# Optimization experiments

Hardware: AMD Instinct MI355X
Metric: run time of the kernel (lower is better)

Reference implementation:

```python
import jax, jax.numpy as jnp
import numpy as np

B, T, J, D, H = 64, 240, 22, 128, 8


def setup_inputs() -> dict:
    key = jax.random.key(0)
    ks = jax.random.split(key, 6)
    x = jax.random.normal(ks[0], (B, T, J, D), dtype=jnp.float32)
    adjacency = jax.random.randint(ks[1], (J, J), 0, 2, dtype=jnp.int32)
    # self-loops so no softmax row is fully masked (matches sane graph usage)
    adjacency = adjacency.at[jnp.arange(J), jnp.arange(J)].set(1)
    in_proj_w = jax.random.normal(ks[2], (3 * D, D), dtype=jnp.float32) * 0.05
    in_proj_b = jax.random.normal(ks[3], (3 * D,), dtype=jnp.float32) * 0.02
    out_w = jax.random.normal(ks[4], (D, D), dtype=jnp.float32) * 0.05
    out_b = jax.random.normal(ks[5], (D,), dtype=jnp.float32) * 0.02
    return {"x": x, "adjacency": adjacency, "in_proj_w": in_proj_w,
            "in_proj_b": in_proj_b, "out_w": out_w, "out_b": out_b}


def reference(x, adjacency, in_proj_w, in_proj_b, out_w, out_b):
    b, t, j, d = x.shape
    hd = d // H
    n = b * t
    x_bt = x.reshape(n, j, d)
    # combined QKV projection (nn.MultiheadAttention in_proj)
    qkv = x_bt @ in_proj_w.T + in_proj_b            # [n, j, 3d]
    q, k, v = jnp.split(qkv, 3, axis=-1)
    split_heads = lambda a: a.reshape(n, j, H, hd).transpose(0, 2, 1, 3)  # [n,H,j,hd]
    q, k, v = split_heads(q), split_heads(k), split_heads(v)
    scores = jnp.einsum('nhqd,nhkd->nhqk', q, k) / np.sqrt(hd).astype(np.float32)
    mask = adjacency <= 0                            # True = disallowed (bool attn_mask)
    scores = jnp.where(mask[None, None], -jnp.inf, scores)
    attn = jax.nn.softmax(scores, axis=-1)
    y = jnp.einsum('nhqk,nhkd->nhqd', attn, v)       # [n,H,j,hd]
    y = y.transpose(0, 2, 1, 3).reshape(n, j, d)
    y = y @ out_w.T + out_b                          # out_proj
    return y.reshape(b, t, j, d)
```

## Files before the change

### kernel.cpp

```cpp
#include <hip/hip_runtime.h>

typedef _Float16 f16;
typedef _Float16 f16x4 __attribute__((ext_vector_type(4)));
typedef _Float16 f16x8 __attribute__((ext_vector_type(8)));
typedef float f32x4 __attribute__((ext_vector_type(4)));

#define N_ROWS   337920
#define TPW      4
#define RG       88
#define NGROUPS  3840

#define QKV_ROWB   512
#define QKV_BYTES  (96 * QKV_ROWB)
#define VT_STRIDE  104
#define LDS_BYTES  (QKV_BYTES + 128 * VT_STRIDE * 2)

__device__ __forceinline__ uint32_t swz(int row, int bytecol) {
  return (uint32_t)((row * QKV_ROWB + bytecol) ^ ((row & 7) << 4));
}

__device__ __forceinline__ f16x8 pack8(float4 a, float4 b) {
  f16x8 r;
  r[0] = (f16)a.x; r[1] = (f16)a.y; r[2] = (f16)a.z; r[3] = (f16)a.w;
  r[4] = (f16)b.x; r[5] = (f16)b.y; r[6] = (f16)b.z; r[7] = (f16)b.w;
  return r;
}

__global__ __launch_bounds__(256, 2)
void mga_fused(const float* __restrict__ x, const int* __restrict__ adj,
               const float* __restrict__ wqkv, const float* __restrict__ bqkv,
               const float* __restrict__ wout, const float* __restrict__ bout,
               float* __restrict__ out) {
  __shared__ __align__(16) char smem[LDS_BYTES];
  char* qkvB = smem;
  f16* vT = (f16*)(smem + QKV_BYTES);

  const int tid  = threadIdx.x;
  const int wv   = tid >> 6;
  const int l    = tid & 63;
  const int g    = l >> 4;
  const int r16  = l & 15;
  const long g0  = (long)blockIdx.x * RG;

  {
    int* p = (int*)vT;
    #pragma unroll
    for (int i = 0; i < 26; i++) p[tid + 256 * i] = 0;
  }

  float mreg[2][2][4];
  #pragma unroll
  for (int qt = 0; qt < 2; qt++)
    #pragma unroll
    for (int jt = 0; jt < 2; jt++)
      #pragma unroll
      for (int r = 0; r < 4; r++) {
        int q = qt * 16 + r16;
        int j = jt * 16 + 4 * g + r;
        float m = -1e30f;
        if (j < 22) {
          if (q >= 22) m = 0.0f;
          else m = (adj[q * 22 + j] > 0) ? 0.0f : -1e30f;
        }
        mreg[qt][jt][r] = m;
      }

  __syncthreads();

  f16x8 bfr[6][4];
  float bias[6];
  #pragma unroll
  for (int i = 0; i < 6; i++) {
    int nt = 6 * wv + i;
    int wrow = nt * 16 + r16;
    const float* wp = wqkv + wrow * 128 + g * 8;
    #pragma unroll
    for (int ks = 0; ks < 4; ks++) {
      float4 u0 = *(const float4*)(wp + ks * 32);
      float4 u1 = *(const float4*)(wp + ks * 32 + 4);
      bfr[i][ks] = pack8(u0, u1);
    }
    bias[i] = bqkv[wrow];
  }

  for (int mt = 0; mt < 6; mt++) {
    long rowg = g0 + mt * 16 + r16;
    if (rowg > (long)N_ROWS - 1) rowg = N_ROWS - 1;
    const float* xp = x + rowg * 128 + g * 8;
    f16x8 afr[4];
    #pragma unroll
    for (int ks = 0; ks < 4; ks++) {
      float4 u0 = *(const float4*)(xp + ks * 32);
      float4 u1 = *(const float4*)(xp + ks * 32 + 4);
      afr[ks] = pack8(u0, u1);
    }
    #pragma unroll
    for (int i = 0; i < 6; i++) {
      f32x4 acc = {0.f, 0.f, 0.f, 0.f};
      #pragma unroll
      for (int ks = 0; ks < 4; ks++)
        acc = __builtin_amdgcn_mfma_f32_16x16x32_f16(afr[ks], bfr[i][ks], acc, 0, 0, 0);
      int nt = 6 * wv + i;
      int col = nt * 16 + r16;
      float b = bias[i];
      float scale = (nt < 8) ? 0.25f : 1.0f;
      #pragma unroll
      for (int r = 0; r < 4; r++) {
        int rowl = mt * 16 + 4 * g + r;
        f16 h = (f16)((acc[r] + b) * scale);
        if (nt < 16) {
          *(f16*)(qkvB + swz(rowl, col * 2)) = h;
        } else {
          int dfull = (nt - 16) * 16 + r16;
          int t = rowl / 22;
          int j = rowl - t * 22;
          vT[dfull * VT_STRIDE + t * 24 + j] = h;
        }
      }
    }
  }
  __syncthreads();

  {
    const int t = wv;
    const int rbase = t * 22;
    for (int h = 0; h < 8; h++) {
      f16x4 kf[2], vf[2];
      #pragma unroll
      for (int jt = 0; jt < 2; jt++) {
        int row = rbase + jt * 16 + r16;
        kf[jt] = *(const f16x4*)(qkvB + swz(row, (128 + h * 16 + 4 * g) * 2));
        vf[jt] = *(const f16x4*)(&vT[(h * 16 + r16) * VT_STRIDE + t * 24 + jt * 16 + 4 * g]);
      }
      #pragma unroll
      for (int qt = 0; qt < 2; qt++) {
        f16x4 qf = *(const f16x4*)(qkvB + swz(rbase + qt * 16 + r16, (h * 16 + 4 * g) * 2));
        f32x4 s0 = {0.f, 0.f, 0.f, 0.f}, s1 = {0.f, 0.f, 0.f, 0.f};
        s0 = __builtin_amdgcn_mfma_f32_16x16x16f16(kf[0], qf, s0, 0, 0, 0);
        s1 = __builtin_amdgcn_mfma_f32_16x16x16f16(kf[1], qf, s1, 0, 0, 0);
        float sv[8];
        #pragma unroll
        for (int r = 0; r < 4; r++) {
          sv[r]     = s0[r] + mreg[qt][0][r];
          sv[4 + r] = s1[r] + mreg[qt][1][r];
        }
        float mx = sv[0];
        #pragma unroll
        for (int i = 1; i < 8; i++) mx = fmaxf(mx, sv[i]);
        mx = fmaxf(mx, __shfl_xor(mx, 16, 64));
        mx = fmaxf(mx, __shfl_xor(mx, 32, 64));
        float p[8], sum = 0.f;
        #pragma unroll
        for (int i = 0; i < 8; i++) { p[i] = __expf(sv[i] - mx); sum += p[i]; }
        sum += __shfl_xor(sum, 16, 64);
        sum += __shfl_xor(sum, 32, 64);
        float inv = 1.0f / sum;
        f16x4 pb0, pb1;
        #pragma unroll
        for (int r = 0; r < 4; r++) {
          pb0[r] = (f16)(p[r] * inv);
          pb1[r] = (f16)(p[4 + r] * inv);
        }
        f32x4 ya = {0.f, 0.f, 0.f, 0.f};
        ya = __builtin_amdgcn_mfma_f32_16x16x16f16(vf[0], pb0, ya, 0, 0, 0);
        ya = __builtin_amdgcn_mfma_f32_16x16x16f16(vf[1], pb1, ya, 0, 0, 0);
        int q = qt * 16 + r16;
        if (q < 22) {
          f16x4 yh;
          #pragma unroll
          for (int r = 0; r < 4; r++) yh[r] = (f16)ya[r];
          *(f16x4*)(qkvB + swz(rbase + q, (h * 16 + 4 * g) * 2)) = yh;
        }
      }
    }
  }
  __syncthreads();

  f16x8 obf[2][4];
  float ob[2];
  #pragma unroll
  for (int i = 0; i < 2; i++) {
    int nt = 2 * wv + i;
    const float* wp = wout + (nt * 16 + r16) * 128 + g * 8;
    #pragma unroll
    for (int ks = 0; ks < 4; ks++) {
      float4 u0 = *(const float4*)(wp + ks * 32);
      float4 u1 = *(const float4*)(wp + ks * 32 + 4);
      obf[i][ks] = pack8(u0, u1);
    }
    ob[i] = bout[nt * 16 + r16];
  }
  for (int mt = 0; mt < 6; mt++) {
    f16x8 afr[4];
    #pragma unroll
    for (int ks = 0; ks < 4; ks++)
      afr[ks] = *(const f16x8*)(qkvB + swz(mt * 16 + r16, (ks * 32 + g * 8) * 2));
    #pragma unroll
    for (int i = 0; i < 2; i++) {
      f32x4 acc = {0.f, 0.f, 0.f, 0.f};
      #pragma unroll
      for (int ks = 0; ks < 4; ks++)
        acc = __builtin_amdgcn_mfma_f32_16x16x32_f16(afr[ks], obf[i][ks], acc, 0, 0, 0);
      int col = (2 * wv + i) * 16 + r16;
      float b = ob[i];
      #pragma unroll
      for (int r = 0; r < 4; r++) {
        int rowl = mt * 16 + 4 * g + r;
        if (rowl < RG) out[(g0 + rowl) * 128 + col] = acc[r] + b;
      }
    }
  }
}

extern "C" void kernel_launch(void* const* d_in, const int* in_sizes, int n_in,
                              void* d_out, int out_size, void* d_ws, size_t ws_size,
                              hipStream_t stream) {
  const float* x    = (const float*)d_in[0];
  const int*   adj  = (const int*)d_in[1];
  const float* wqkv = (const float*)d_in[2];
  const float* bqkv = (const float*)d_in[3];
  const float* wout = (const float*)d_in[4];
  const float* bout = (const float*)d_in[5];
  float* o = (float*)d_out;
  mga_fused<<<dim3(NGROUPS), dim3(256), 0, stream>>>(x, adj, wqkv, bqkv, wout, bout, o);
}
```

Measured before the change: 277.3 us.

## Halve rows per block, pre-convert weights to f16, swap MFMA operands for vector stores

Each block now handles 2 timesteps (44 rows) instead of 4, with 7680 blocks and a smaller LDS footprint, so 4 blocks can run per CU instead of 2. A small pre-kernel converts the QKV and output weights to f16 in the workspace, so each block loads half as many weight bytes and skips the per-block conversion. The MFMA operands are swapped so each lane holds 4 consecutive output columns, which allows f16x4 LDS writes and float4 global stores. Attention work is split per wave by timestep and head-half, and V-transpose gets a new swizzle. The cost is an extra kernel launch and more clamped or padded rows per block.

```diff
diff --git a/kernel.cpp b/kernel.cpp
--- a/kernel.cpp
+++ b/kernel.cpp
@@ -6,17 +6,21 @@
 typedef float f32x4 __attribute__((ext_vector_type(4)));
 
 #define N_ROWS   337920
-#define TPW      4
-#define RG       88
-#define NGROUPS  3840
-
-#define QKV_ROWB   512
-#define QKV_BYTES  (96 * QKV_ROWB)
-#define VT_STRIDE  104
-#define LDS_BYTES  (QKV_BYTES + 128 * VT_STRIDE * 2)
+#define RG       44
+#define NGROUPS  7680
+#define QKV_ROWB  512
+#define QKV_BYTES (48 * QKV_ROWB)
+#define VT_OFF    QKV_BYTES
+#define LDS_BYTES (QKV_BYTES + 128 * 64 * 2)
+
+#define WQKV_F16_ELEMS 49152
+#define WS_NEEDED ((49152 + 16384) * 2)
 
 __device__ __forceinline__ uint32_t swz(int row, int bytecol) {
   return (uint32_t)((row * QKV_ROWB + bytecol) ^ ((row & 7) << 4));
+}
+__device__ __forceinline__ uint32_t vswz(int d, int col) {
+  return (uint32_t)(VT_OFF + ((d * 128 + col * 2) ^ ((d & 15) << 3)));
 }
 
 __device__ __forceinline__ f16x8 pack8(float4 a, float4 b) {
@@ -26,26 +30,96 @@
   return r;
 }
 
-__global__ __launch_bounds__(256, 2)
+__device__ __forceinline__ f16x8 ldw8(const f16* w16p, const float* w32p, int f16m) {
+  if (f16m) return *(const f16x8*)w16p;
+  float4 u0 = *(const float4*)w32p;
+  float4 u1 = *(const float4*)(w32p + 4);
+  return pack8(u0, u1);
+}
+
+__global__ void prep_w(const float* __restrict__ wqkv, const float* __restrict__ wout,
+                       f16* __restrict__ w16) {
+  int i4 = (blockIdx.x * 256 + threadIdx.x) * 4;
+  const float* src = (i4 < WQKV_F16_ELEMS) ? (wqkv + i4) : (wout + (i4 - WQKV_F16_ELEMS));
+  float4 v = *(const float4*)src;
+  f16x4 h;
+  h[0] = (f16)v.x; h[1] = (f16)v.y; h[2] = (f16)v.z; h[3] = (f16)v.w;
+  *(f16x4*)(w16 + i4) = h;
+}
+
+__global__ __launch_bounds__(256, 4)
 void mga_fused(const float* __restrict__ x, const int* __restrict__ adj,
-               const float* __restrict__ wqkv, const float* __restrict__ bqkv,
-               const float* __restrict__ wout, const float* __restrict__ bout,
+               const float* __restrict__ bqkv, const float* __restrict__ bout,
+               const f16* __restrict__ w16, const float* __restrict__ wqkv32,
+               const float* __restrict__ wout32, int f16m,
                float* __restrict__ out) {
   __shared__ __align__(16) char smem[LDS_BYTES];
-  char* qkvB = smem;
-  f16* vT = (f16*)(smem + QKV_BYTES);
-
-  const int tid  = threadIdx.x;
-  const int wv   = tid >> 6;
-  const int l    = tid & 63;
-  const int g    = l >> 4;
-  const int r16  = l & 15;
-  const long g0  = (long)blockIdx.x * RG;
+
+  const int tid = threadIdx.x;
+  const int wv  = tid >> 6;
+  const int l   = tid & 63;
+  const int g   = l >> 4;
+  const int r16 = l & 15;
+  const long g0 = (long)blockIdx.x * RG;
 
   {
-    int* p = (int*)vT;
-    #pragma unroll
-    for (int i = 0; i < 26; i++) p[tid + 256 * i] = 0;
+    int* p = (int*)(smem + VT_OFF);
+    #pragma unroll
+    for (int i = 0; i < 16; i++) p[tid + 256 * i] = 0;
+  }
+  __syncthreads();
+
+  f16x8 xf[3][4];
+  #pragma unroll
+  for (int mt = 0; mt < 3; mt++) {
+    long rowg = g0 + mt * 16 + r16;
+    if (rowg > (long)N_ROWS - 1) rowg = N_ROWS - 1;
+    const float* xp = x + rowg * 128 + g * 8;
+    #pragma unroll
+    for (int ks = 0; ks < 4; ks++) {
+      float4 u0 = *(const float4*)(xp + ks * 32);
+      float4 u1 = *(const float4*)(xp + ks * 32 + 4);
+      xf[mt][ks] = pack8(u0, u1);
+    }
+  }
+
+  #pragma unroll
+  for (int i = 0; i < 6; i++) {
+    int nt = wv + 4 * i;
+    int wrow = nt * 16 + r16;
+    f16x8 wf[4];
+    #pragma unroll
+    for (int ks = 0; ks < 4; ks++) {
+      int off = wrow * 128 + ks * 32 + g * 8;
+      wf[ks] = ldw8(w16 + off, wqkv32 + off, f16m);
+    }
+    float4 bv = *(const float4*)(bqkv + nt * 16 + 4 * g);
+    float scale = (nt < 8) ? 0.25f : 1.0f;
+    f32x4 acc[3] = {{0,0,0,0},{0,0,0,0},{0,0,0,0}};
+    #pragma unroll
+    for (int mt = 0; mt < 3; mt++)
+      #pragma unroll
+      for (int ks = 0; ks < 4; ks++)
+        acc[mt] = __builtin_amdgcn_mfma_f32_16x16x32_f16(wf[ks], xf[mt][ks], acc[mt], 0, 0, 0);
+
+    #pragma unroll
+    for (int mt = 0; mt < 3; mt++) {
+      int rowl = mt * 16 + r16;
+      if (nt < 16) {
+        f16x4 h4;
+        #pragma unroll
+        for (int r = 0; r < 4; r++) h4[r] = (f16)((acc[mt][r] + ((const float*)&bv)[r]) * scale);
+        *(f16x4*)(smem + swz(rowl, (nt * 16 + 4 * g) * 2)) = h4;
+      } else if (rowl < RG) {
+        int t = rowl >= 22;
+        int j = rowl - 22 * t;
+        int col = t * 32 + j;
+        int dv = (nt - 16) * 16 + 4 * g;
+        #pragma unroll
+        for (int r = 0; r < 4; r++)
+          *(f16*)(smem + vswz(dv + r, col)) = (f16)(acc[mt][r] + ((const float*)&bv)[r]);
+      }
+    }
   }
 
   float mreg[2][2][4];
@@ -58,84 +132,31 @@
         int q = qt * 16 + r16;
         int j = jt * 16 + 4 * g + r;
         float m = -1e30f;
-        if (j < 22) {
-          if (q >= 22) m = 0.0f;
-          else m = (adj[q * 22 + j] > 0) ? 0.0f : -1e30f;
-        }
+        if (j < 22) m = (q >= 22 || adj[q * 22 + j] > 0) ? 0.0f : -1e30f;
         mreg[qt][jt][r] = m;
       }
 
   __syncthreads();
 
-  f16x8 bfr[6][4];
-  float bias[6];
-  #pragma unroll
-  for (int i = 0; i < 6; i++) {
-    int nt = 6 * wv + i;
-    int wrow = nt * 16 + r16;
-    const float* wp = wqkv + wrow * 128 + g * 8;
-    #pragma unroll
-    for (int ks = 0; ks < 4; ks++) {
-      float4 u0 = *(const float4*)(wp + ks * 32);
-      float4 u1 = *(const float4*)(wp + ks * 32 + 4);
-      bfr[i][ks] = pack8(u0, u1);
-    }
-    bias[i] = bqkv[wrow];
-  }
-
-  for (int mt = 0; mt < 6; mt++) {
-    long rowg = g0 + mt * 16 + r16;
-    if (rowg > (long)N_ROWS - 1) rowg = N_ROWS - 1;
-    const float* xp = x + rowg * 128 + g * 8;
-    f16x8 afr[4];
-    #pragma unroll
-    for (int ks = 0; ks < 4; ks++) {
-      float4 u0 = *(const float4*)(xp + ks * 32);
-      float4 u1 = *(const float4*)(xp + ks * 32 + 4);
-      afr[ks] = pack8(u0, u1);
-    }
-    #pragma unroll
-    for (int i = 0; i < 6; i++) {
-      f32x4 acc = {0.f, 0.f, 0.f, 0.f};
-      #pragma unroll
-      for (int ks = 0; ks < 4; ks++)
-        acc = __builtin_amdgcn_mfma_f32_16x16x32_f16(afr[ks], bfr[i][ks], acc, 0, 0, 0);
-      int nt = 6 * wv + i;
-      int col = nt * 16 + r16;
-      float b = bias[i];
-      float scale = (nt < 8) ? 0.25f : 1.0f;
-      #pragma unroll
-      for (int r = 0; r < 4; r++) {
-        int rowl = mt * 16 + 4 * g + r;
-        f16 h = (f16)((acc[r] + b) * scale);
-        if (nt < 16) {
-          *(f16*)(qkvB + swz(rowl, col * 2)) = h;
-        } else {
-          int dfull = (nt - 16) * 16 + r16;
-          int t = rowl / 22;
-          int j = rowl - t * 22;
-          vT[dfull * VT_STRIDE + t * 24 + j] = h;
-        }
-      }
-    }
-  }
-  __syncthreads();
-
   {
-    const int t = wv;
-    const int rbase = t * 22;
-    for (int h = 0; h < 8; h++) {
+    const int t = wv >> 1;
+    const int rbase = 22 * t;
+    for (int hi = 0; hi < 4; hi++) {
+      int h = 4 * (wv & 1) + hi;
       f16x4 kf[2], vf[2];
       #pragma unroll
       for (int jt = 0; jt < 2; jt++) {
-        int row = rbase + jt * 16 + r16;
-        kf[jt] = *(const f16x4*)(qkvB + swz(row, (128 + h * 16 + 4 * g) * 2));
-        vf[jt] = *(const f16x4*)(&vT[(h * 16 + r16) * VT_STRIDE + t * 24 + jt * 16 + 4 * g]);
+        int rowk = rbase + jt * 16 + r16;
+        if (rowk > 47) rowk = 47;
+        kf[jt] = *(const f16x4*)(smem + swz(rowk, (128 + h * 16 + 4 * g) * 2));
+        vf[jt] = *(const f16x4*)(smem + vswz(h * 16 + r16, t * 32 + jt * 16 + 4 * g));
       }
       #pragma unroll
       for (int qt = 0; qt < 2; qt++) {
-        f16x4 qf = *(const f16x4*)(qkvB + swz(rbase + qt * 16 + r16, (h * 16 + 4 * g) * 2));
-        f32x4 s0 = {0.f, 0.f, 0.f, 0.f}, s1 = {0.f, 0.f, 0.f, 0.f};
+        int rowq = rbase + qt * 16 + r16;
+        if (rowq > 47) rowq = 47;
+        f16x4 qf = *(const f16x4*)(smem + swz(rowq, (h * 16 + 4 * g) * 2));
+        f32x4 s0 = {0.f,0.f,0.f,0.f}, s1 = {0.f,0.f,0.f,0.f};
         s0 = __builtin_amdgcn_mfma_f32_16x16x16f16(kf[0], qf, s0, 0, 0, 0);
         s1 = __builtin_amdgcn_mfma_f32_16x16x16f16(kf[1], qf, s1, 0, 0, 0);
         float sv[8];
@@ -161,7 +182,7 @@
           pb0[r] = (f16)(p[r] * inv);
           pb1[r] = (f16)(p[4 + r] * inv);
         }
-        f32x4 ya = {0.f, 0.f, 0.f, 0.f};
+        f32x4 ya = {0.f,0.f,0.f,0.f};
         ya = __builtin_amdgcn_mfma_f32_16x16x16f16(vf[0], pb0, ya, 0, 0, 0);
         ya = __builtin_amdgcn_mfma_f32_16x16x16f16(vf[1], pb1, ya, 0, 0, 0);
         int q = qt * 16 + r16;
@@ -169,44 +190,44 @@
           f16x4 yh;
           #pragma unroll
           for (int r = 0; r < 4; r++) yh[r] = (f16)ya[r];
-          *(f16x4*)(qkvB + swz(rbase + q, (h * 16 + 4 * g) * 2)) = yh;
+          *(f16x4*)(smem + swz(rbase + q, (h * 16 + 4 * g) * 2)) = yh;
         }
       }
     }
   }
   __syncthreads();
 
-  f16x8 obf[2][4];
-  float ob[2];
+  const f16* w16o = w16 + WQKV_F16_ELEMS;
+  f16x8 wf[2][4];
+  float4 bv[2];
   #pragma unroll
   for (int i = 0; i < 2; i++) {
     int nt = 2 * wv + i;
-    const float* wp = wout + (nt * 16 + r16) * 128 + g * 8;
+    int wrow = nt * 16 + r16;
     #pragma unroll
     for (int ks = 0; ks < 4; ks++) {
-      float4 u0 = *(const float4*)(wp + ks * 32);
-      float4 u1 = *(const float4*)(wp + ks * 32 + 4);
-      obf[i][ks] = pack8(u0, u1);
-    }
-    ob[i] = bout[nt * 16 + r16];
-  }
-  for (int mt = 0; mt < 6; mt++) {
-    f16x8 afr[4];
+      int off = wrow * 128 + ks * 32 + g * 8;
+      wf[i][ks] = ldw8(w16o + off, wout32 + off, f16m);
+    }
+    bv[i] = *(const float4*)(bout + nt * 16 + 4 * g);
+  }
+  for (int mt = 0; mt < 3; mt++) {
+    f16x8 af[4];
     #pragma unroll
     for (int ks = 0; ks < 4; ks++)
-      afr[ks] = *(const f16x8*)(qkvB + swz(mt * 16 + r16, (ks * 32 + g * 8) * 2));
+      af[ks] = *(const f16x8*)(smem + swz(mt * 16 + r16, (ks * 32 + g * 8) * 2));
+    int rowl = mt * 16 + r16;
     #pragma unroll
     for (int i = 0; i < 2; i++) {
-      f32x4 acc = {0.f, 0.f, 0.f, 0.f};
+      f32x4 acc = {0.f,0.f,0.f,0.f};
       #pragma unroll
       for (int ks = 0; ks < 4; ks++)
-        acc = __builtin_amdgcn_mfma_f32_16x16x32_f16(afr[ks], obf[i][ks], acc, 0, 0, 0);
-      int col = (2 * wv + i) * 16 + r16;
-      float b = ob[i];
-      #pragma unroll
-      for (int r = 0; r < 4; r++) {
-        int rowl = mt * 16 + 4 * g + r;
-        if (rowl < RG) out[(g0 + rowl) * 128 + col] = acc[r] + b;
+        acc = __builtin_amdgcn_mfma_f32_16x16x32_f16(wf[i][ks], af[ks], acc, 0, 0, 0);
+      if (rowl < RG) {
+        float4 o;
+        o.x = acc[0] + bv[i].x; o.y = acc[1] + bv[i].y;
+        o.z = acc[2] + bv[i].z; o.w = acc[3] + bv[i].w;
+        *(float4*)(out + (g0 + rowl) * 128 + (2 * wv + i) * 16 + 4 * g) = o;
       }
     }
   }
@@ -222,5 +243,10 @@
   const float* wout = (const float*)d_in[4];
   const float* bout = (const float*)d_in[5];
   float* o = (float*)d_out;
-  mga_fused<<<dim3(NGROUPS), dim3(256), 0, stream>>>(x, adj, wqkv, bqkv, wout, bout, o);
-}
+
+  int f16m = (d_ws != nullptr && ws_size >= (size_t)WS_NEEDED) ? 1 : 0;
+  f16* w16 = (f16*)d_ws;
+  if (f16m) prep_w<<<dim3(64), dim3(256), 0, stream>>>(wqkv, wout, w16);
+  mga_fused<<<dim3(NGROUPS), dim3(256), 0, stream>>>(x, adj, bqkv, bout,
+                                                     w16, wqkv, wout, f16m, o);
+}
```

Result: faster. 260.5 us (-6.1%).
